# Kernel optimization log

Hardware: AMD Instinct MI355X
Metric: run time of the kernel (lower is better)

The kernel has to match this reference:

```python
import jax, jax.numpy as jnp
import numpy as np

WIDTH = [512, 512, 512, 512]
GRID_SIZE = 5
K = 3  # spline order
GRID_RANGE = (-1.0, 1.0)
BATCH = 1024


def extend_grid(grid, k):
    # grid: (I, G+1) -> (I, G+2k+1), extend k knots on each side with uniform step h
    h = (grid[:, -1:] - grid[:, :1]) / (grid.shape[1] - 1)
    for _ in range(k):
        grid = jnp.concatenate([grid[:, :1] - h, grid, grid[:, -1:] + h], axis=1)
    return grid


def b_spline_basis(x, grid, k):
    # Cox-de Boor recursion. x: (B, I), grid: (I, G+2k+1) -> (B, I, G+k)
    xe = x[:, :, None]
    g = grid[None, :, :]
    B = ((xe >= g[:, :, :-1]) & (xe < g[:, :, 1:])).astype(x.dtype)
    for p in range(1, k + 1):
        B = ((xe - g[:, :, :-(p + 1)]) / (g[:, :, p:-1] - g[:, :, :-(p + 1)]) * B[:, :, :-1]
             + (g[:, :, p + 1:] - xe) / (g[:, :, p + 1:] - g[:, :, 1:-p]) * B[:, :, 1:])
    return B


def kan_layer(x, grid, coef, sb, sp):
    # x: (B, I); coef: (I, O, G+k); sb, sp: (I, O)
    base = jax.nn.silu(x)                              # residual b(x), (B, I)
    Bmat = b_spline_basis(x, grid, K)                  # (B, I, G+k)
    y = jnp.einsum('bik,iok->bio', Bmat, coef)         # spline curves, (B, I, O)
    post = sb[None] * base[:, :, None] + sp[None] * y  # postacts (B, I, O)
    return post.sum(axis=1)                            # (B, O)


def setup_inputs() -> dict:
    key = jax.random.key(0)
    ks = jax.random.split(key, 1 + 2 * (len(WIDTH) - 1))
    inp = {"x": jax.random.normal(ks[0], (BATCH, WIDTH[0]), dtype=jnp.float32)}
    for l, (i, o) in enumerate(zip(WIDTH[:-1], WIDTH[1:])):
        base = jnp.linspace(GRID_RANGE[0], GRID_RANGE[1], GRID_SIZE + 1, dtype=jnp.float32)
        grid = extend_grid(jnp.broadcast_to(base[None], (i, GRID_SIZE + 1)), K)
        kc, kb = ks[1 + 2 * l], ks[2 + 2 * l]
        inp[f"grid{l}"] = grid
        inp[f"coef{l}"] = jax.random.normal(kc, (i, o, GRID_SIZE + K), dtype=jnp.float32) * (0.1 / GRID_SIZE)
        inp[f"sb{l}"] = (jax.random.uniform(kb, (i, o), dtype=jnp.float32) * 2.0 - 1.0) / np.sqrt(i).astype(np.float32)
        inp[f"sp{l}"] = jnp.ones((i, o), dtype=jnp.float32) / np.sqrt(i).astype(np.float32)
    return inp


def reference(x, grid0, coef0, sb0, sp0, grid1, coef1, sb1, sp1, grid2, coef2, sb2, sp2):
    x = kan_layer(x, grid0, coef0, sb0, sp0)
    x = kan_layer(x, grid1, coef1, sb1, sp1)
    x = kan_layer(x, grid2, coef2, sb2, sp2)
    return x
```

## Files before the change

### kernel.cpp

```cpp
#include <hip/hip_runtime.h>
#include <hip/hip_bf16.h>

#define I_DIM  512
#define O_DIM  512
#define NBATCH 1024
#define NSPL   8
#define KPI    12
#define KDIM   (I_DIM * KPI)
#define NGRID  12

#define SPLITK 4
#define KSEG   (KDIM / SPLITK)
#define BK     128
#define BM     64
#define BN     64

typedef __attribute__((ext_vector_type(8))) short bf16x8;
typedef __attribute__((ext_vector_type(4))) float f32x4;

__device__ __forceinline__ void gload_lds16(const __hip_bfloat16* g, __hip_bfloat16* l) {
    __builtin_amdgcn_global_load_lds(
        (const __attribute__((address_space(1))) void*)g,
        (__attribute__((address_space(3))) void*)l, 16, 0, 0);
}

__device__ __forceinline__ void features_core(float xv, const float* __restrict__ grid,
                                              __hip_bfloat16* __restrict__ dst) {
    float g[NGRID];
#pragma unroll
    for (int j = 0; j < NGRID; ++j) g[j] = grid[j];

    float h  = g[1] - g[0];
    float r1 = 1.0f / h;
    float r2 = 1.0f / (2.0f * h);
    float r3 = 1.0f / (3.0f * h);

    float B[NGRID - 1];
#pragma unroll
    for (int j = 0; j < NGRID - 1; ++j)
        B[j] = (xv >= g[j] && xv < g[j + 1]) ? 1.0f : 0.0f;

#pragma unroll
    for (int j = 0; j < NGRID - 2; ++j)
        B[j] = (xv - g[j]) * r1 * B[j] + (g[j + 2] - xv) * r1 * B[j + 1];
#pragma unroll
    for (int j = 0; j < NGRID - 3; ++j)
        B[j] = (xv - g[j]) * r2 * B[j] + (g[j + 3] - xv) * r2 * B[j + 1];
#pragma unroll
    for (int j = 0; j < NGRID - 4; ++j)
        B[j] = (xv - g[j]) * r3 * B[j] + (g[j + 4] - xv) * r3 * B[j + 1];

    float s = xv / (1.0f + __expf(-xv));
    __hip_bfloat16 shi = __float2bfloat16(s);
    __hip_bfloat16 slo = __float2bfloat16(s - __bfloat162float(shi));

    __align__(16) __hip_bfloat16 row[KPI];
#pragma unroll
    for (int k = 0; k < NSPL; ++k) row[k] = __float2bfloat16(B[k]);
    row[8]  = shi;
    row[9]  = shi;
    row[10] = slo;
    row[11] = __float2bfloat16(0.0f);

    uint2* d = (uint2*)dst;
    const uint2* srow = (const uint2*)row;
    d[0] = srow[0]; d[1] = srow[1]; d[2] = srow[2];
}

__device__ __forceinline__ void wt_row_core(const float* __restrict__ coef,
                                            const float* __restrict__ sb,
                                            const float* __restrict__ sp,
                                            int i, int o,
                                            __hip_bfloat16* __restrict__ W) {
    float sbv = sb[i * O_DIM + o];
    float spv = sp[i * O_DIM + o];
    const float* cf = coef + (size_t)(i * O_DIM + o) * NSPL;
    __align__(16) __hip_bfloat16 row[KPI];
#pragma unroll
    for (int k = 0; k < NSPL; ++k) row[k] = __float2bfloat16(spv * cf[k]);
    __hip_bfloat16 whi = __float2bfloat16(sbv);
    __hip_bfloat16 wlo = __float2bfloat16(sbv - __bfloat162float(whi));
    row[8]  = whi;
    row[9]  = wlo;
    row[10] = whi;
    row[11] = __float2bfloat16(0.0f);
    uint2* dst = (uint2*)(W + (size_t)o * KDIM + i * KPI);
    const uint2* src = (const uint2*)row;
    dst[0] = src[0]; dst[1] = src[1]; dst[2] = src[2];
}

#define WT_BLOCKS   3072
#define FEAT_BLOCKS 2048
__global__ __launch_bounds__(256)
void prep_kernel(const float* __restrict__ x0, const float* __restrict__ gr0,
                 const float* __restrict__ c0, const float* __restrict__ sb0, const float* __restrict__ sp0,
                 const float* __restrict__ c1, const float* __restrict__ sb1, const float* __restrict__ sp1,
                 const float* __restrict__ c2, const float* __restrict__ sb2, const float* __restrict__ sp2,
                 __hip_bfloat16* __restrict__ Wt,
                 __hip_bfloat16* __restrict__ F) {
    int b = blockIdx.x;
    int t = threadIdx.x;
    if (b < WT_BLOCKS) {
        int l   = b >> 10;
        int rem = b & 1023;
        int i0  = (rem & 7) * 64;
        int o0  = (rem >> 3) * 4;
        const float* coef = l == 0 ? c0  : (l == 1 ? c1  : c2);
        const float* sb   = l == 0 ? sb0 : (l == 1 ? sb1 : sb2);
        const float* sp   = l == 0 ? sp0 : (l == 1 ? sp1 : sp2);
        wt_row_core(coef, sb, sp, i0 + (t >> 2), o0 + (t & 3),
                    Wt + (size_t)l * O_DIM * KDIM);
    } else {
        int e = (b - WT_BLOCKS) * 256 + t;
        features_core(x0[e], gr0, F + (size_t)e * KPI);
    }
}

__global__ __launch_bounds__(256)
void build_features_sum(const float* __restrict__ P,
                        const float* __restrict__ grid,
                        __hip_bfloat16* __restrict__ F) {
    int e0 = (blockIdx.x * blockDim.x + threadIdx.x) * 4;
    f32x4 xv = (f32x4){0.f, 0.f, 0.f, 0.f};
#pragma unroll
    for (int s = 0; s < SPLITK; ++s) {
        f32x4 v = *(const f32x4*)&P[(size_t)s * NBATCH * I_DIM + e0];
        xv.x += v.x; xv.y += v.y; xv.z += v.z; xv.w += v.w;
    }
    features_core(xv.x, grid, F + (size_t)(e0 + 0) * KPI);
    features_core(xv.y, grid, F + (size_t)(e0 + 1) * KPI);
    features_core(xv.z, grid, F + (size_t)(e0 + 2) * KPI);
    features_core(xv.w, grid, F + (size_t)(e0 + 3) * KPI);
}

__global__ __launch_bounds__(256)
void reduce_out(const float* __restrict__ P, float* __restrict__ out) {
    int e0 = (blockIdx.x * blockDim.x + threadIdx.x) * 4;
    f32x4 v0 = (f32x4){0.f, 0.f, 0.f, 0.f};
#pragma unroll
    for (int s = 0; s < SPLITK; ++s) {
        f32x4 v = *(const f32x4*)&P[(size_t)s * NBATCH * O_DIM + e0];
        v0.x += v.x; v0.y += v.y; v0.z += v.z; v0.w += v.w;
    }
    *(f32x4*)&out[e0] = v0;
}

__global__ __launch_bounds__(256)
void gemm_kernel(const __hip_bfloat16* __restrict__ A,
                 const __hip_bfloat16* __restrict__ Wt,
                 float* __restrict__ P) {
    __shared__ __hip_bfloat16 lA[BM * BK];
    __shared__ __hip_bfloat16 lB[BN * BK];

    int bm = blockIdx.x;
    int bn = blockIdx.y;
    int ks = blockIdx.z;
    int tid = threadIdx.x;
    int lane = tid & 63;
    int wave = tid >> 6;
    int wr = (wave & 1) * 32;
    int wc = (wave >> 1) * 32;
    int q  = lane >> 4;
    int ln = lane & 15;

    f32x4 acc[2][2];
#pragma unroll
    for (int a = 0; a < 2; ++a)
#pragma unroll
        for (int b = 0; b < 2; ++b) acc[a][b] = (f32x4){0.f, 0.f, 0.f, 0.f};

    const __hip_bfloat16* Abase = A  + (size_t)(bm * BM) * KDIM + ks * KSEG;
    const __hip_bfloat16* Bbase = Wt + (size_t)(bn * BN) * KDIM + ks * KSEG;

    for (int kt = 0; kt < KSEG; kt += BK) {
        __syncthreads();
#pragma unroll
        for (int c = 0; c < 4; ++c) {
            int cc = wave * 256 + c * 64 + lane;
            int r = cc >> 4, j = (cc & 15) ^ (r & 7);
            gload_lds16(Abase + (size_t)r * KDIM + kt + j * 8,
                        lA + (size_t)(wave * 256 + c * 64) * 8);
        }
#pragma unroll
        for (int c = 0; c < 4; ++c) {
            int cc = wave * 256 + c * 64 + lane;
            int r = cc >> 4, j = (cc & 15) ^ (r & 7);
            gload_lds16(Bbase + (size_t)r * KDIM + kt + j * 8,
                        lB + (size_t)(wave * 256 + c * 64) * 8);
        }
        __syncthreads();

#pragma unroll
        for (int kh = 0; kh < 4; ++kh) {
            bf16x8 af[2], bfr[2];
#pragma unroll
            for (int rt = 0; rt < 2; ++rt) {
                int row = wr + rt * 16 + ln;
                af[rt] = *(const bf16x8*)(lA + row * BK + (((kh * 4 + q) ^ (row & 7)) * 8));
            }
#pragma unroll
            for (int ct = 0; ct < 2; ++ct) {
                int row = wc + ct * 16 + ln;
                bfr[ct] = *(const bf16x8*)(lB + row * BK + (((kh * 4 + q) ^ (row & 7)) * 8));
            }
#pragma unroll
            for (int rt = 0; rt < 2; ++rt)
#pragma unroll
                for (int ct = 0; ct < 2; ++ct)
                    acc[rt][ct] = __builtin_amdgcn_mfma_f32_16x16x32_bf16(
                        af[rt], bfr[ct], acc[rt][ct], 0, 0, 0);
        }
    }

    float* Pp = P + (size_t)ks * NBATCH * O_DIM;
    int orow = bm * BM + wr;
    int ocol = bn * BN + wc + ln;
#pragma unroll
    for (int rt = 0; rt < 2; ++rt)
#pragma unroll
        for (int ct = 0; ct < 2; ++ct)
#pragma unroll
            for (int r = 0; r < 4; ++r)
                Pp[(size_t)(orow + rt * 16 + q * 4 + r) * O_DIM + ocol + ct * 16]
                    = acc[rt][ct][r];
}

extern "C" void kernel_launch(void* const* d_in, const int* in_sizes, int n_in,
                              void* d_out, int out_size, void* d_ws, size_t ws_size,
                              hipStream_t stream) {
    const float* x0  = (const float*)d_in[0];
    const float* gr0 = (const float*)d_in[1];
    const float* c0  = (const float*)d_in[2];
    const float* sb0 = (const float*)d_in[3];
    const float* sp0 = (const float*)d_in[4];
    const float* gr1 = (const float*)d_in[5];
    const float* c1  = (const float*)d_in[6];
    const float* sb1 = (const float*)d_in[7];
    const float* sp1 = (const float*)d_in[8];
    const float* gr2 = (const float*)d_in[9];
    const float* c2  = (const float*)d_in[10];
    const float* sb2 = (const float*)d_in[11];
    const float* sp2 = (const float*)d_in[12];

    char* ws = (char*)d_ws;
    const size_t wt_bytes = (size_t)O_DIM * KDIM * sizeof(__hip_bfloat16);
    const size_t f_bytes  = (size_t)NBATCH * KDIM * sizeof(__hip_bfloat16);
    __hip_bfloat16* Wt = (__hip_bfloat16*)ws;
    __hip_bfloat16* F  = (__hip_bfloat16*)(ws + 3 * wt_bytes);
    float* P = (float*)(ws + 3 * wt_bytes + f_bytes);
    float* out = (float*)d_out;

    prep_kernel<<<WT_BLOCKS + FEAT_BLOCKS, 256, 0, stream>>>(
        x0, gr0, c0, sb0, sp0, c1, sb1, sp1, c2, sb2, sp2, Wt, F);

    gemm_kernel<<<dim3(NBATCH / BM, O_DIM / BN, SPLITK), 256, 0, stream>>>(F, Wt, P);

    build_features_sum<<<(NBATCH * I_DIM) / 1024, 256, 0, stream>>>(P, gr1, F);
    gemm_kernel<<<dim3(NBATCH / BM, O_DIM / BN, SPLITK), 256, 0, stream>>>(
        F, Wt + (size_t)O_DIM * KDIM, P);

    build_features_sum<<<(NBATCH * I_DIM) / 1024, 256, 0, stream>>>(P, gr2, F);
    gemm_kernel<<<dim3(NBATCH / BM, O_DIM / BN, SPLITK), 256, 0, stream>>>(
        F, Wt + (size_t)2 * O_DIM * KDIM, P);

    reduce_out<<<(NBATCH * O_DIM) / 1024, 256, 0, stream>>>(P, out);
}
```

Measured before the change: 175.7 us.

## Double-buffer LDS tiles in split-K GEMM to overlap loads with MFMA

```diff
diff --git a/kernel.cpp b/kernel.cpp
--- a/kernel.cpp
+++ b/kernel.cpp
@@ -14,6 +14,7 @@
 #define BK     128
 #define BM     64
 #define BN     64
+#define NT     (KSEG / BK)
 
 typedef __attribute__((ext_vector_type(8))) short bf16x8;
 typedef __attribute__((ext_vector_type(4))) float f32x4;
@@ -149,8 +150,8 @@
 void gemm_kernel(const __hip_bfloat16* __restrict__ A,
                  const __hip_bfloat16* __restrict__ Wt,
                  float* __restrict__ P) {
-    __shared__ __hip_bfloat16 lA[BM * BK];
-    __shared__ __hip_bfloat16 lB[BN * BK];
+    __shared__ __hip_bfloat16 lA[2][BM * BK];
+    __shared__ __hip_bfloat16 lB[2][BN * BK];
 
     int bm = blockIdx.x;
     int bn = blockIdx.y;
@@ -172,45 +173,77 @@
     const __hip_bfloat16* Abase = A  + (size_t)(bm * BM) * KDIM + ks * KSEG;
     const __hip_bfloat16* Bbase = Wt + (size_t)(bn * BN) * KDIM + ks * KSEG;
 
-    for (int kt = 0; kt < KSEG; kt += BK) {
-        __syncthreads();
-#pragma unroll
-        for (int c = 0; c < 4; ++c) {
-            int cc = wave * 256 + c * 64 + lane;
-            int r = cc >> 4, j = (cc & 15) ^ (r & 7);
-            gload_lds16(Abase + (size_t)r * KDIM + kt + j * 8,
-                        lA + (size_t)(wave * 256 + c * 64) * 8);
+    size_t goff[4];
+    int    loff[4];
+#pragma unroll
+    for (int c = 0; c < 4; ++c) {
+        int cc = wave * 256 + c * 64 + lane;
+        int r = cc >> 4, j = (cc & 15) ^ (r & 7);
+        goff[c] = (size_t)r * KDIM + j * 8;
+        loff[c] = (wave * 256 + c * 64) * 8;
+    }
+
+#define STAGE(buf, kt)                                                        \
+    do {                                                                      \
+        _Pragma("unroll")                                                     \
+        for (int c = 0; c < 4; ++c)                                           \
+            gload_lds16(Abase + goff[c] + (kt), &lA[buf][loff[c]]);           \
+        _Pragma("unroll")                                                     \
+        for (int c = 0; c < 4; ++c)                                           \
+            gload_lds16(Bbase + goff[c] + (kt), &lB[buf][loff[c]]);           \
+    } while (0)
+
+#define COMPUTE(buf)                                                          \
+    do {                                                                      \
+        _Pragma("unroll")                                                     \
+        for (int kh = 0; kh < 4; ++kh) {                                      \
+            bf16x8 af[2], bfr[2];                                             \
+            _Pragma("unroll")                                                 \
+            for (int rt = 0; rt < 2; ++rt) {                                  \
+                int row = wr + rt * 16 + ln;                                  \
+                af[rt] = *(const bf16x8*)(&lA[buf][0] + row * BK +            \
+                                          (((kh * 4 + q) ^ (row & 7)) * 8));  \
+            }                                                                 \
+            _Pragma("unroll")                                                 \
+            for (int ct = 0; ct < 2; ++ct) {                                  \
+                int row = wc + ct * 16 + ln;                                  \
+                bfr[ct] = *(const bf16x8*)(&lB[buf][0] + row * BK +           \
+                                           (((kh * 4 + q) ^ (row & 7)) * 8)); \
+            }                                                                 \
+            _Pragma("unroll")                                                 \
+            for (int rt = 0; rt < 2; ++rt)                                    \
+                _Pragma("unroll")                                             \
+                for (int ct = 0; ct < 2; ++ct)                                \
+                    acc[rt][ct] = __builtin_amdgcn_mfma_f32_16x16x32_bf16(    \
+                        af[rt], bfr[ct], acc[rt][ct], 0, 0, 0);               \
+        }                                                                     \
+    } while (0)
+
+    STAGE(0, 0);
+    STAGE(1, BK);
+
+    for (int t = 0; t < NT; t += 2) {
+        asm volatile("s_waitcnt vmcnt(8)" ::: "memory");
+        __builtin_amdgcn_s_barrier();
+        __builtin_amdgcn_sched_barrier(0);
+        COMPUTE(0);
+        __builtin_amdgcn_s_barrier();
+        __builtin_amdgcn_sched_barrier(0);
+        if (t + 2 < NT) STAGE(0, (t + 2) * BK);
+        if (t + 3 < NT) {
+            asm volatile("s_waitcnt vmcnt(8)" ::: "memory");
+        } else {
+            asm volatile("s_waitcnt vmcnt(0)" ::: "memory");
         }
-#pragma unroll
-        for (int c = 0; c < 4; ++c) {
-            int cc = wave * 256 + c * 64 + lane;
-            int r = cc >> 4, j = (cc & 15) ^ (r & 7);
-            gload_lds16(Bbase + (size_t)r * KDIM + kt + j * 8,
-                        lB + (size_t)(wave * 256 + c * 64) * 8);
-        }
-        __syncthreads();
-
-#pragma unroll
-        for (int kh = 0; kh < 4; ++kh) {
-            bf16x8 af[2], bfr[2];
-#pragma unroll
-            for (int rt = 0; rt < 2; ++rt) {
-                int row = wr + rt * 16 + ln;
-                af[rt] = *(const bf16x8*)(lA + row * BK + (((kh * 4 + q) ^ (row & 7)) * 8));
-            }
-#pragma unroll
-            for (int ct = 0; ct < 2; ++ct) {
-                int row = wc + ct * 16 + ln;
-                bfr[ct] = *(const bf16x8*)(lB + row * BK + (((kh * 4 + q) ^ (row & 7)) * 8));
-            }
-#pragma unroll
-            for (int rt = 0; rt < 2; ++rt)
-#pragma unroll
-                for (int ct = 0; ct < 2; ++ct)
-                    acc[rt][ct] = __builtin_amdgcn_mfma_f32_16x16x32_bf16(
-                        af[rt], bfr[ct], acc[rt][ct], 0, 0, 0);
-        }
-    }
+        __builtin_amdgcn_s_barrier();
+        __builtin_amdgcn_sched_barrier(0);
+        COMPUTE(1);
+        __builtin_amdgcn_s_barrier();
+        __builtin_amdgcn_sched_barrier(0);
+        if (t + 3 < NT) STAGE(1, (t + 3) * BK);
+    }
+#undef STAGE
+#undef COMPUTE
 
     float* Pp = P + (size_t)ks * NBATCH * O_DIM;
     int orow = bm * BM + wr;
```

New measurement: 169.8 us (median of 2 runs). 1.03x faster.
